# Kernel tuning notes

Hardware: AMD Instinct MI355X
Metric: run time of the kernel (lower is better)

Reference implementation:

```python
import jax, jax.numpy as jnp
import numpy as np

B, T = 64, 262144

def setup_inputs() -> dict:
    key = jax.random.key(0)
    ks = jax.random.split(key, 6)
    x = jax.random.normal(ks[0], (B, T, 1), dtype=jnp.float32)
    # b's ~ U(-1, 1); a's ~ U(-0.5, 0.5) per DTDFIICell init
    b0 = jax.random.uniform(ks[1], (1,), dtype=jnp.float32, minval=-1.0, maxval=1.0)
    b1 = jax.random.uniform(ks[2], (1,), dtype=jnp.float32, minval=-1.0, maxval=1.0)
    b2 = jax.random.uniform(ks[3], (1,), dtype=jnp.float32, minval=-1.0, maxval=1.0)
    a1 = jax.random.uniform(ks[4], (1,), dtype=jnp.float32, minval=-0.5, maxval=0.5)
    a2 = jax.random.uniform(ks[5], (1,), dtype=jnp.float32, minval=-0.5, maxval=0.5)
    return {"x": x, "b0": b0, "b1": b1, "b2": b2, "a1": a1, "a2": a2}

def reference(x, b0, b1, b2, a1, a2):
    # x: [B, T, 1]; Direct-Form-II biquad recurrence over T.
    batch = x.shape[0]
    xs = jnp.transpose(x[:, :, 0])  # [T, B] time-major for scan

    def step(v, xt):
        # v: [B, 2] delay-line state; xt: [B]
        out = xt * b0 + v[:, 0]
        v_new = jnp.stack(
            [xt * b1 + v[:, 1] - out * a1,
             xt * b2 - out * a2], axis=-1)
        return v_new, out

    v0 = jnp.zeros((batch, 2), dtype=x.dtype)
    _, outs = jax.lax.scan(step, v0, xs)  # outs: [T, B]
    return jnp.transpose(outs)[:, :, None]  # [B, T, 1]
```

## Files before the change

### kernel.cpp

```cpp
#include <hip/hip_runtime.h>


constexpr int BATCH = 64;
constexpr int T_LEN = 262144;
constexpr int TPB   = 256;
constexpr int LPT   = 32;
constexpr int TILE  = TPB * LPT;
constexpr int NBPB  = T_LEN / TILE;
constexpr int NB    = BATCH * NBPB;
constexpr int WUP   = 4096;
constexpr int WPT   = WUP / TPB;

typedef float vfloat4 __attribute__((ext_vector_type(4)));

#define MATSQ(m00, m01, m10, m11)                                  \
    {                                                              \
        float n00 = fmaf(m00, m00, m01 * m10);                     \
        float n01 = fmaf(m00, m01, m01 * m11);                     \
        float n10 = fmaf(m10, m00, m11 * m10);                     \
        float n11 = fmaf(m10, m01, m11 * m11);                     \
        m00 = n00; m01 = n01; m10 = n10; m11 = n11;                \
    }

#define CSTEP(p0, p1, xa, xb, xc, xd)                                        \
    {                                                                        \
        float n0 = fmaf(q00, p0, fmaf(q01, p1,                               \
                   fmaf(k3_0, (xa), fmaf(k2_0, (xb),                         \
                   fmaf(k1_0, (xc), c0 * (xd))))));                          \
        float n1 = fmaf(q10, p0, fmaf(q11, p1,                               \
                   fmaf(k3_1, (xa), fmaf(k2_1, (xb),                         \
                   fmaf(k1_1, (xc), c1 * (xd))))));                          \
        p0 = n0; p1 = n1;                                                    \
    }

__global__ __launch_bounds__(TPB, 4) void biquad_trunc(
    const float* __restrict__ x, float* __restrict__ out,
    const float* __restrict__ pb0, const float* __restrict__ pb1,
    const float* __restrict__ pb2, const float* __restrict__ pa1,
    const float* __restrict__ pa2)
{
    __shared__ float lds[TPB][LPT + 1];
    __shared__ float swv[16];

    const int tid  = threadIdx.x;
    const int lane = tid & 63;
    const int w    = tid >> 6;
    const int g    = blockIdx.x;
    const int b    = g >> 5;
    const int k    = g & (NBPB - 1);

    const float b0 = *pb0, b1 = *pb1, b2 = *pb2;
    const float a1 = *pa1, a2 = *pa2;
    const float na1 = -a1, na2 = -a2;

    const float c0 = fmaf(na1, b0, b1), c1 = fmaf(na2, b0, b2);
    const float A00 = na1, A01 = 1.f, A10 = na2, A11 = 0.f;
    const float k1_0 = fmaf(A00, c0, A01 * c1);
    const float k1_1 = fmaf(A10, c0, A11 * c1);
    float B00 = A00, B01 = A01, B10 = A10, B11 = A11;
    MATSQ(B00, B01, B10, B11);
    const float k2_0 = fmaf(B00, c0, B01 * c1);
    const float k2_1 = fmaf(B10, c0, B11 * c1);
    const float k3_0 = fmaf(B00, k1_0, B01 * k1_1);
    const float k3_1 = fmaf(B10, k1_0, B11 * k1_1);
    float q00 = B00, q01 = B01, q10 = B10, q11 = B11;
    MATSQ(q00, q01, q10, q11);

    const size_t base = (size_t)b * T_LEN + (size_t)k * TILE;

    float4 wq[4];
    if (k > 0) {
        const float4* wsrc =
            reinterpret_cast<const float4*>(x + base - WUP) + tid * (WPT / 4);
#pragma unroll
        for (int i = 0; i < 4; ++i) wq[i] = wsrc[i];
    }

    const float4* src = reinterpret_cast<const float4*>(x + base);
#pragma unroll
    for (int it = 0; it < 8; ++it) {
        int idx = it * TPB + tid;
        float4 v = src[idx];
        int e = idx * 4, c = e >> 5, t = e & 31;
        lds[c][t] = v.x; lds[c][t + 1] = v.y;
        lds[c][t + 2] = v.z; lds[c][t + 3] = v.w;
    }

    float pA0 = 0.f, pA1 = 0.f;
    if (k > 0) {
#pragma unroll
        for (int i = 0; i < 4; ++i)
            CSTEP(pA0, pA1, wq[i].x, wq[i].y, wq[i].z, wq[i].w);
    }
    __syncthreads();

    float xv[LPT];
#pragma unroll
    for (int t = 0; t < LPT; ++t) xv[t] = lds[tid][t];

    float pB0 = 0.f, pB1 = 0.f;
#pragma unroll
    for (int i = 0; i < LPT / 4; ++i)
        CSTEP(pB0, pB1, xv[4 * i], xv[4 * i + 1], xv[4 * i + 2], xv[4 * i + 3]);

    float wa00 = q00, wa01 = q01, wa10 = q10, wa11 = q11;
    MATSQ(wa00, wa01, wa10, wa11);
    MATSQ(wa00, wa01, wa10, wa11);
    float m00 = wa00, m01 = wa01, m10 = wa10, m11 = wa11;
    MATSQ(m00, m01, m10, m11);
    float wb00 = m00, wb01 = m01, wb10 = m10, wb11 = m11;

    for (int d = 1; d < 64; d <<= 1) {
        float oA0 = __shfl_up(pA0, d), oA1 = __shfl_up(pA1, d);
        float oB0 = __shfl_up(pB0, d), oB1 = __shfl_up(pB1, d);
        if (lane >= d) {
            pA0 = fmaf(wa00, oA0, fmaf(wa01, oA1, pA0));
            pA1 = fmaf(wa10, oA0, fmaf(wa11, oA1, pA1));
            pB0 = fmaf(wb00, oB0, fmaf(wb01, oB1, pB0));
            pB1 = fmaf(wb10, oB0, fmaf(wb11, oB1, pB1));
        }
        MATSQ(wa00, wa01, wa10, wa11);
        MATSQ(wb00, wb01, wb10, wb11);
    }

    float einB0 = __shfl_up(pB0, 1);
    float einB1 = __shfl_up(pB1, 1);
    if (lane == 0) { einB0 = 0.f; einB1 = 0.f; }

    if (lane == 63) {
        swv[2 * w] = pA0;     swv[2 * w + 1] = pA1;
        swv[8 + 2 * w] = pB0; swv[9 + 2 * w] = pB1;
    }
    __syncthreads();

    float sA0 = 0.f, sA1 = 0.f;
#pragma unroll
    for (int u = 0; u < 4; ++u) {
        float t0 = fmaf(wa00, sA0, fmaf(wa01, sA1, swv[2 * u]));
        float t1 = fmaf(wa10, sA0, fmaf(wa11, sA1, swv[2 * u + 1]));
        sA0 = t0; sA1 = t1;
    }
    float cw0 = 0.f, cw1 = 0.f;
    for (int u = 0; u < w; ++u) {
        float t0 = fmaf(wb00, cw0, fmaf(wb01, cw1, swv[8 + 2 * u]));
        float t1 = fmaf(wb10, cw0, fmaf(wb11, cw1, swv[9 + 2 * u]));
        cw0 = t0; cw1 = t1;
    }

    float vs0 = sA0, vs1 = sA1;
    float vc0 = cw0, vc1 = cw1;
    {
        float t00 = m00, t01 = m01, t10 = m10, t11 = m11;
#pragma unroll
        for (int bit = 0; bit < 8; ++bit) {
            if ((tid >> bit) & 1) {
                float n0 = fmaf(t00, vs0, t01 * vs1);
                float n1 = fmaf(t10, vs0, t11 * vs1);
                vs0 = n0; vs1 = n1;
                if (bit < 6) {
                    float u0 = fmaf(t00, vc0, t01 * vc1);
                    float u1 = fmaf(t10, vc0, t11 * vc1);
                    vc0 = u0; vc1 = u1;
                }
            }
            MATSQ(t00, t01, t10, t11);
        }
    }
    float v0 = vs0 + vc0 + einB0;
    float v1 = vs1 + vc1 + einB1;

    float o2 = fmaf(xv[0], b0, v0);
    float vn0 = fmaf(na1, o2, fmaf(xv[0], b1, v1));
    float o1 = fmaf(xv[1], b0, vn0);
    lds[tid][0] = o2; lds[tid][1] = o1;
#pragma unroll
    for (int t = 2; t < LPT; ++t) {
        float acc = fmaf(b1, xv[t - 1], fmaf(b2, xv[t - 2], na2 * o2));
        float o   = fmaf(b0, xv[t], fmaf(na1, o1, acc));
        lds[tid][t] = o;
        o2 = o1; o1 = o;
    }
    __syncthreads();

    vfloat4* dst = reinterpret_cast<vfloat4*>(out + base);
#pragma unroll
    for (int it = 0; it < 8; ++it) {
        int idx = it * TPB + tid;
        int e = idx * 4, c = e >> 5, t = e & 31;
        vfloat4 v;
        v.x = lds[c][t];     v.y = lds[c][t + 1];
        v.z = lds[c][t + 2]; v.w = lds[c][t + 3];
        __builtin_nontemporal_store(v, &dst[idx]);
    }
}

extern "C" void kernel_launch(void* const* d_in, const int* in_sizes, int n_in,
                              void* d_out, int out_size, void* d_ws, size_t ws_size,
                              hipStream_t stream) {
    const float* x   = (const float*)d_in[0];
    const float* pb0 = (const float*)d_in[1];
    const float* pb1 = (const float*)d_in[2];
    const float* pb2 = (const float*)d_in[3];
    const float* pa1 = (const float*)d_in[4];
    const float* pa2 = (const float*)d_in[5];
    float* out = (float*)d_out;

    biquad_trunc<<<NB, TPB, 0, stream>>>(x, out, pb0, pb1, pb2, pa1, pa2);
}
```

Measured before the change: 30.59 us.

## Process two consecutive tiles per block to halve warm-up overhead

After: 32.02 us. +4.6%, slower.

```diff
diff --git a/kernel.cpp b/kernel.cpp
--- a/kernel.cpp
+++ b/kernel.cpp
@@ -6,10 +6,10 @@
 constexpr int TPB   = 256;
 constexpr int LPT   = 32;
 constexpr int TILE  = TPB * LPT;
-constexpr int NBPB  = T_LEN / TILE;
+constexpr int SPAN  = 2 * TILE;
+constexpr int NBPB  = T_LEN / SPAN;
 constexpr int NB    = BATCH * NBPB;
 constexpr int WUP   = 4096;
-constexpr int WPT   = WUP / TPB;
 
 typedef float vfloat4 __attribute__((ext_vector_type(4)));
 
@@ -33,20 +33,21 @@
         p0 = n0; p1 = n1;                                                    \
     }
 
-__global__ __launch_bounds__(TPB, 4) void biquad_trunc(
+__global__ __launch_bounds__(TPB, 2) void biquad_2tile(
     const float* __restrict__ x, float* __restrict__ out,
     const float* __restrict__ pb0, const float* __restrict__ pb1,
     const float* __restrict__ pb2, const float* __restrict__ pa1,
     const float* __restrict__ pa2)
 {
-    __shared__ float lds[TPB][LPT + 1];
-    __shared__ float swv[16];
+    __shared__ float ldsA[TPB][LPT + 1];
+    __shared__ float ldsB[TPB][LPT + 1];
+    __shared__ float swv[24];
 
     const int tid  = threadIdx.x;
     const int lane = tid & 63;
     const int w    = tid >> 6;
     const int g    = blockIdx.x;
-    const int b    = g >> 5;
+    const int b    = g >> 4;
     const int k    = g & (NBPB - 1);
 
     const float b0 = *pb0, b1 = *pb1, b2 = *pb2;
@@ -66,131 +67,195 @@
     float q00 = B00, q01 = B01, q10 = B10, q11 = B11;
     MATSQ(q00, q01, q10, q11);
 
-    const size_t base = (size_t)b * T_LEN + (size_t)k * TILE;
+    const size_t base = (size_t)b * T_LEN + (size_t)k * SPAN;
 
     float4 wq[4];
     if (k > 0) {
-        const float4* wsrc =
-            reinterpret_cast<const float4*>(x + base - WUP) + tid * (WPT / 4);
+        const float4* wsrc = reinterpret_cast<const float4*>(x + base - WUP) + tid * 4;
 #pragma unroll
         for (int i = 0; i < 4; ++i) wq[i] = wsrc[i];
     }
-
-    const float4* src = reinterpret_cast<const float4*>(x + base);
-#pragma unroll
-    for (int it = 0; it < 8; ++it) {
-        int idx = it * TPB + tid;
-        float4 v = src[idx];
-        int e = idx * 4, c = e >> 5, t = e & 31;
-        lds[c][t] = v.x; lds[c][t + 1] = v.y;
-        lds[c][t + 2] = v.z; lds[c][t + 3] = v.w;
-    }
-
+    const float4* srcA = reinterpret_cast<const float4*>(x + base);
+    const float4* srcB = srcA + TILE / 4;
+
+#pragma unroll
+    for (int it = 0; it < 8; ++it) {
+        int idx = it * TPB + tid;
+        float4 v = srcA[idx];
+        int e = idx * 4, c = e >> 5, t = e & 31;
+        ldsA[c][t] = v.x; ldsA[c][t + 1] = v.y;
+        ldsA[c][t + 2] = v.z; ldsA[c][t + 3] = v.w;
+    }
+#pragma unroll
+    for (int it = 0; it < 8; ++it) {
+        int idx = it * TPB + tid;
+        float4 v = srcB[idx];
+        int e = idx * 4, c = e >> 5, t = e & 31;
+        ldsB[c][t] = v.x; ldsB[c][t + 1] = v.y;
+        ldsB[c][t + 2] = v.z; ldsB[c][t + 3] = v.w;
+    }
+    __syncthreads();
+
+    float xv[LPT];
+#pragma unroll
+    for (int t = 0; t < LPT; ++t) xv[t] = ldsA[tid][t];
+
+    float pW0 = 0.f, pW1 = 0.f;
+    if (k > 0) {
+#pragma unroll
+        for (int i = 0; i < 4; ++i)
+            CSTEP(pW0, pW1, wq[i].x, wq[i].y, wq[i].z, wq[i].w);
+    }
     float pA0 = 0.f, pA1 = 0.f;
-    if (k > 0) {
-#pragma unroll
-        for (int i = 0; i < 4; ++i)
-            CSTEP(pA0, pA1, wq[i].x, wq[i].y, wq[i].z, wq[i].w);
-    }
-    __syncthreads();
-
-    float xv[LPT];
-#pragma unroll
-    for (int t = 0; t < LPT; ++t) xv[t] = lds[tid][t];
-
+#pragma unroll
+    for (int i = 0; i < LPT / 4; ++i)
+        CSTEP(pA0, pA1, xv[4 * i], xv[4 * i + 1], xv[4 * i + 2], xv[4 * i + 3]);
     float pB0 = 0.f, pB1 = 0.f;
 #pragma unroll
     for (int i = 0; i < LPT / 4; ++i)
-        CSTEP(pB0, pB1, xv[4 * i], xv[4 * i + 1], xv[4 * i + 2], xv[4 * i + 3]);
-
-    float wa00 = q00, wa01 = q01, wa10 = q10, wa11 = q11;
-    MATSQ(wa00, wa01, wa10, wa11);
-    MATSQ(wa00, wa01, wa10, wa11);
-    float m00 = wa00, m01 = wa01, m10 = wa10, m11 = wa11;
+        CSTEP(pB0, pB1, ldsB[tid][4 * i], ldsB[tid][4 * i + 1],
+                        ldsB[tid][4 * i + 2], ldsB[tid][4 * i + 3]);
+
+    float wW00 = q00, wW01 = q01, wW10 = q10, wW11 = q11;
+    MATSQ(wW00, wW01, wW10, wW11);
+    MATSQ(wW00, wW01, wW10, wW11);
+    float m00 = wW00, m01 = wW01, m10 = wW10, m11 = wW11;
     MATSQ(m00, m01, m10, m11);
-    float wb00 = m00, wb01 = m01, wb10 = m10, wb11 = m11;
+    float wM00 = m00, wM01 = m01, wM10 = m10, wM11 = m11;
 
     for (int d = 1; d < 64; d <<= 1) {
+        float oW0 = __shfl_up(pW0, d), oW1 = __shfl_up(pW1, d);
         float oA0 = __shfl_up(pA0, d), oA1 = __shfl_up(pA1, d);
         float oB0 = __shfl_up(pB0, d), oB1 = __shfl_up(pB1, d);
         if (lane >= d) {
-            pA0 = fmaf(wa00, oA0, fmaf(wa01, oA1, pA0));
-            pA1 = fmaf(wa10, oA0, fmaf(wa11, oA1, pA1));
-            pB0 = fmaf(wb00, oB0, fmaf(wb01, oB1, pB0));
-            pB1 = fmaf(wb10, oB0, fmaf(wb11, oB1, pB1));
-        }
-        MATSQ(wa00, wa01, wa10, wa11);
-        MATSQ(wb00, wb01, wb10, wb11);
-    }
-
-    float einB0 = __shfl_up(pB0, 1);
-    float einB1 = __shfl_up(pB1, 1);
-    if (lane == 0) { einB0 = 0.f; einB1 = 0.f; }
+            pW0 = fmaf(wW00, oW0, fmaf(wW01, oW1, pW0));
+            pW1 = fmaf(wW10, oW0, fmaf(wW11, oW1, pW1));
+            pA0 = fmaf(wM00, oA0, fmaf(wM01, oA1, pA0));
+            pA1 = fmaf(wM10, oA0, fmaf(wM11, oA1, pA1));
+            pB0 = fmaf(wM00, oB0, fmaf(wM01, oB1, pB0));
+            pB1 = fmaf(wM10, oB0, fmaf(wM11, oB1, pB1));
+        }
+        MATSQ(wW00, wW01, wW10, wW11);
+        MATSQ(wM00, wM01, wM10, wM11);
+    }
+
+    float einA0 = __shfl_up(pA0, 1), einA1 = __shfl_up(pA1, 1);
+    float einB0 = __shfl_up(pB0, 1), einB1 = __shfl_up(pB1, 1);
+    if (lane == 0) { einA0 = einA1 = einB0 = einB1 = 0.f; }
 
     if (lane == 63) {
-        swv[2 * w] = pA0;     swv[2 * w + 1] = pA1;
-        swv[8 + 2 * w] = pB0; swv[9 + 2 * w] = pB1;
+        swv[6 * w]     = pW0; swv[6 * w + 1] = pW1;
+        swv[6 * w + 2] = pA0; swv[6 * w + 3] = pA1;
+        swv[6 * w + 4] = pB0; swv[6 * w + 5] = pB1;
     }
     __syncthreads();
 
     float sA0 = 0.f, sA1 = 0.f;
 #pragma unroll
     for (int u = 0; u < 4; ++u) {
-        float t0 = fmaf(wa00, sA0, fmaf(wa01, sA1, swv[2 * u]));
-        float t1 = fmaf(wa10, sA0, fmaf(wa11, sA1, swv[2 * u + 1]));
+        float t0 = fmaf(wW00, sA0, fmaf(wW01, sA1, swv[6 * u]));
+        float t1 = fmaf(wW10, sA0, fmaf(wW11, sA1, swv[6 * u + 1]));
         sA0 = t0; sA1 = t1;
     }
-    float cw0 = 0.f, cw1 = 0.f;
+    float agA0 = 0.f, agA1 = 0.f;
+#pragma unroll
+    for (int u = 0; u < 4; ++u) {
+        float t0 = fmaf(wM00, agA0, fmaf(wM01, agA1, swv[6 * u + 2]));
+        float t1 = fmaf(wM10, agA0, fmaf(wM11, agA1, swv[6 * u + 3]));
+        agA0 = t0; agA1 = t1;
+    }
+    float cwA0 = 0.f, cwA1 = 0.f, cwB0 = 0.f, cwB1 = 0.f;
     for (int u = 0; u < w; ++u) {
-        float t0 = fmaf(wb00, cw0, fmaf(wb01, cw1, swv[8 + 2 * u]));
-        float t1 = fmaf(wb10, cw0, fmaf(wb11, cw1, swv[9 + 2 * u]));
-        cw0 = t0; cw1 = t1;
-    }
-
-    float vs0 = sA0, vs1 = sA1;
-    float vc0 = cw0, vc1 = cw1;
+        float t0 = fmaf(wM00, cwA0, fmaf(wM01, cwA1, swv[6 * u + 2]));
+        float t1 = fmaf(wM10, cwA0, fmaf(wM11, cwA1, swv[6 * u + 3]));
+        cwA0 = t0; cwA1 = t1;
+        float u0 = fmaf(wM00, cwB0, fmaf(wM01, cwB1, swv[6 * u + 4]));
+        float u1 = fmaf(wM10, cwB0, fmaf(wM11, cwB1, swv[6 * u + 5]));
+        cwB0 = u0; cwB1 = u1;
+    }
+    float P00 = wM00, P01 = wM01, P10 = wM10, P11 = wM11;
+    MATSQ(P00, P01, P10, P11);
+    MATSQ(P00, P01, P10, P11);
+    float sB0 = fmaf(P00, sA0, fmaf(P01, sA1, agA0));
+    float sB1 = fmaf(P10, sA0, fmaf(P11, sA1, agA1));
+
+    float vA0 = sA0, vA1 = sA1, vB0 = sB0, vB1 = sB1;
+    float vcA0 = cwA0, vcA1 = cwA1, vcB0 = cwB0, vcB1 = cwB1;
     {
         float t00 = m00, t01 = m01, t10 = m10, t11 = m11;
 #pragma unroll
         for (int bit = 0; bit < 8; ++bit) {
             if ((tid >> bit) & 1) {
-                float n0 = fmaf(t00, vs0, t01 * vs1);
-                float n1 = fmaf(t10, vs0, t11 * vs1);
-                vs0 = n0; vs1 = n1;
+                float n0, n1;
+                n0 = fmaf(t00, vA0, t01 * vA1); n1 = fmaf(t10, vA0, t11 * vA1);
+                vA0 = n0; vA1 = n1;
+                n0 = fmaf(t00, vB0, t01 * vB1); n1 = fmaf(t10, vB0, t11 * vB1);
+                vB0 = n0; vB1 = n1;
                 if (bit < 6) {
-                    float u0 = fmaf(t00, vc0, t01 * vc1);
-                    float u1 = fmaf(t10, vc0, t11 * vc1);
-                    vc0 = u0; vc1 = u1;
+                    n0 = fmaf(t00, vcA0, t01 * vcA1); n1 = fmaf(t10, vcA0, t11 * vcA1);
+                    vcA0 = n0; vcA1 = n1;
+                    n0 = fmaf(t00, vcB0, t01 * vcB1); n1 = fmaf(t10, vcB0, t11 * vcB1);
+                    vcB0 = n0; vcB1 = n1;
                 }
             }
             MATSQ(t00, t01, t10, t11);
         }
     }
-    float v0 = vs0 + vc0 + einB0;
-    float v1 = vs1 + vc1 + einB1;
-
-    float o2 = fmaf(xv[0], b0, v0);
-    float vn0 = fmaf(na1, o2, fmaf(xv[0], b1, v1));
-    float o1 = fmaf(xv[1], b0, vn0);
-    lds[tid][0] = o2; lds[tid][1] = o1;
-#pragma unroll
-    for (int t = 2; t < LPT; ++t) {
-        float acc = fmaf(b1, xv[t - 1], fmaf(b2, xv[t - 2], na2 * o2));
-        float o   = fmaf(b0, xv[t], fmaf(na1, o1, acc));
-        lds[tid][t] = o;
-        o2 = o1; o1 = o;
+    float v0 = vA0 + vcA0 + einA0;
+    float v1 = vA1 + vcA1 + einA1;
+    float u0 = vB0 + vcB0 + einB0;
+    float u1 = vB1 + vcB1 + einB1;
+
+    {
+        float o2 = fmaf(xv[0], b0, v0);
+        float vn0 = fmaf(na1, o2, fmaf(xv[0], b1, v1));
+        float o1 = fmaf(xv[1], b0, vn0);
+        ldsA[tid][0] = o2; ldsA[tid][1] = o1;
+#pragma unroll
+        for (int t = 2; t < LPT; ++t) {
+            float acc = fmaf(b1, xv[t - 1], fmaf(b2, xv[t - 2], na2 * o2));
+            float o   = fmaf(b0, xv[t], fmaf(na1, o1, acc));
+            ldsA[tid][t] = o;
+            o2 = o1; o1 = o;
+        }
+    }
+    {
+        float xm2 = ldsB[tid][0], xm1 = ldsB[tid][1];
+        float o2 = fmaf(xm2, b0, u0);
+        float vn0 = fmaf(na1, o2, fmaf(xm2, b1, u1));
+        float o1 = fmaf(xm1, b0, vn0);
+        ldsB[tid][0] = o2; ldsB[tid][1] = o1;
+#pragma unroll
+        for (int t = 2; t < LPT; ++t) {
+            float xt  = ldsB[tid][t];
+            float acc = fmaf(b1, xm1, fmaf(b2, xm2, na2 * o2));
+            float o   = fmaf(b0, xt, fmaf(na1, o1, acc));
+            ldsB[tid][t] = o;
+            xm2 = xm1; xm1 = xt;
+            o2 = o1; o1 = o;
+        }
     }
     __syncthreads();
 
-    vfloat4* dst = reinterpret_cast<vfloat4*>(out + base);
+    vfloat4* dstA = reinterpret_cast<vfloat4*>(out + base);
+    vfloat4* dstB = dstA + TILE / 4;
 #pragma unroll
     for (int it = 0; it < 8; ++it) {
         int idx = it * TPB + tid;
         int e = idx * 4, c = e >> 5, t = e & 31;
         vfloat4 v;
-        v.x = lds[c][t];     v.y = lds[c][t + 1];
-        v.z = lds[c][t + 2]; v.w = lds[c][t + 3];
-        __builtin_nontemporal_store(v, &dst[idx]);
+        v.x = ldsA[c][t];     v.y = ldsA[c][t + 1];
+        v.z = ldsA[c][t + 2]; v.w = ldsA[c][t + 3];
+        __builtin_nontemporal_store(v, &dstA[idx]);
+    }
+#pragma unroll
+    for (int it = 0; it < 8; ++it) {
+        int idx = it * TPB + tid;
+        int e = idx * 4, c = e >> 5, t = e & 31;
+        vfloat4 v;
+        v.x = ldsB[c][t];     v.y = ldsB[c][t + 1];
+        v.z = ldsB[c][t + 2]; v.w = ldsB[c][t + 3];
+        __builtin_nontemporal_store(v, &dstB[idx]);
     }
 }
 
@@ -205,5 +270,5 @@
     const float* pa2 = (const float*)d_in[5];
     float* out = (float*)d_out;
 
-    biquad_trunc<<<NB, TPB, 0, stream>>>(x, out, pb0, pb1, pb2, pa1, pa2);
+    biquad_2tile<<<NB, TPB, 0, stream>>>(x, out, pb0, pb1, pb2, pa1, pa2);
 }
```
